# Kernel optimization log

Measured on AMD Instinct MI355X. Metric: run time of the kernel, lower is better.

## Reference

```python
import jax, jax.numpy as jnp
import numpy as np

CODEBOOK_SIZE = 4096
EMBED_DIM = 256
BETA = 0.25


def setup_inputs() -> dict:
    key = jax.random.key(0)
    k_z, k_cb = jax.random.split(key)
    z = jax.random.normal(k_z, (32, 256, 32, 32), dtype=jnp.float32)
    # nn.Embedding weight init: uniform(-1/D, 1/D)
    codebook = jax.random.uniform(
        k_cb, (CODEBOOK_SIZE, EMBED_DIM), dtype=jnp.float32,
        minval=-1.0 / EMBED_DIM, maxval=1.0 / EMBED_DIM)
    return {"z": z, "codebook": codebook}


def reference(z, codebook):
    b, c, h, w = z.shape
    # (B,C,H,W) -> (B*H*W, D)
    z_flat = jnp.transpose(z, (0, 2, 3, 1)).reshape(-1, c)
    # squared euclidean distances: ||z||^2 - 2 z.e^T + ||e||^2  (== cdist(...)^2)
    z_sq = jnp.sum(z_flat * z_flat, axis=1, keepdims=True)          # (N,1)
    e_sq = jnp.sum(codebook * codebook, axis=1)                     # (K,)
    distances = z_sq - 2.0 * (z_flat @ codebook.T) + e_sq[None, :]  # (N,K)
    min_encoding_indices = jnp.argmin(distances, axis=1)            # (N,)
    z_q_flat = codebook[min_encoding_indices]                       # (N,D)
    z_q = jnp.transpose(z_q_flat.reshape(b, h, w, c), (0, 3, 1, 2))  # (B,C,H,W)
    # straight-through estimator
    z_q_st = z + jax.lax.stop_gradient(z_q - z)
    codebook_loss = jnp.mean((z_q - jax.lax.stop_gradient(z)) ** 2)
    commitment_loss = jnp.mean((z - jax.lax.stop_gradient(z_q)) ** 2)
    vq_loss = codebook_loss + BETA * commitment_loss
    return (z_q_st, vq_loss, min_encoding_indices.reshape(b, h, w))
```

## Files before the change

kernel.cpp:

```cpp
#include <hip/hip_runtime.h>

#define K_CODES 4096
#define D 256
#define N_VEC 32768
#define N_ELEM 8388608
#define WINDOW 3.5e-4f
#define RG 8
#define RSLICE 256

typedef _Float16 f16x8 __attribute__((ext_vector_type(8)));
typedef float f32x4 __attribute__((ext_vector_type(4)));

#define WS_LOSS 0
#define WS_COUNT 8
#define WS_DONE 16
#define WS_IDX 256
#define WS_LIST (WS_IDX + N_VEC * 4)
#define WS_ESQ (WS_LIST + N_VEC * 4)
#define WS_ZSQ (WS_ESQ + K_CODES * 4)
#define WS_APACK (WS_ZSQ + N_VEC * 4)
#define WS_BPACK (WS_APACK + (size_t)N_VEC * 256 * 2)
#define WS_RFIN (WS_BPACK + (size_t)K_CODES * 256 * 2 + 65536)

#define PREP_PZ 4096
#define PREP_PCB 512
#define PREP_ESQ 1024
#define PREP_ZSQ 128
#define PREP_BLOCKS (PREP_PZ + PREP_PCB + PREP_ESQ + PREP_ZSQ)

__device__ __forceinline__ unsigned long long pack_key(float s, int idx) {
  const unsigned u = __float_as_uint(s);
  const unsigned mk = (u & 0x80000000u) ? ~u : (u | 0x80000000u);
  return ((unsigned long long)mk << 12) | (unsigned long long)(unsigned)idx;
}
__device__ __forceinline__ float key_score(unsigned long long k) {
  const unsigned mk = (unsigned)(k >> 12);
  const unsigned u = (mk & 0x80000000u) ? (mk & 0x7fffffffu) : ~mk;
  return __uint_as_float(u);
}

__device__ __forceinline__ void pin_frag(f16x8& v) {
  asm volatile("" : "+v"(v));
}

__device__ void esq_body(int bx, const float* __restrict__ cb,
                         float* __restrict__ esq) {
  const int lane = threadIdx.x & 63;
  const int k = bx * 4 + (threadIdx.x >> 6);
  const float* row = cb + (size_t)k * D;
  double s = 0.;
#pragma unroll
  for (int j = 0; j < 4; ++j) {
    const float v = row[lane + 64 * j];
    s += (double)__fmul_rn(v, v);
  }
#pragma unroll
  for (int off = 32; off > 0; off >>= 1) s += __shfl_down(s, off, 64);
  if (lane == 0) esq[k] = (float)s;
}

__device__ void zsq_body(int bx, const float* __restrict__ z,
                         float* __restrict__ zsq) {
  const int n = bx * 256 + threadIdx.x;
  const int b = n >> 10;
  const int hw = n & 1023;
  const float* p = z + ((size_t)b << 18) + hw;
  double a0 = 0., a1 = 0., a2 = 0., a3 = 0.;
  for (int c = 0; c < D; c += 4) {
    const float v0 = p[(size_t)(c + 0) << 10];
    const float v1 = p[(size_t)(c + 1) << 10];
    const float v2 = p[(size_t)(c + 2) << 10];
    const float v3 = p[(size_t)(c + 3) << 10];
    a0 += (double)__fmul_rn(v0, v0);
    a1 += (double)__fmul_rn(v1, v1);
    a2 += (double)__fmul_rn(v2, v2);
    a3 += (double)__fmul_rn(v3, v3);
  }
  zsq[n] = (float)((a0 + a1) + (a2 + a3));
}

__device__ void pack_z2_body(int bx, const float* __restrict__ z,
                             _Float16* __restrict__ Ap) {
  const int t = bx * 256 + threadIdx.x;
  const int lane = t & 63;
  const int fid = t >> 6;
  const int ks = fid & 7;
  const int grp = fid >> 3;
  const int n = grp * 16 + (lane & 15);
  const int d = ks * 32 + ((lane >> 4) << 3);
  const int b = n >> 10, hw = n & 1023;
  const float* p = z + ((size_t)b << 18) + ((size_t)d << 10) + hw;
  f16x8 H;
#pragma unroll
  for (int j = 0; j < 8; ++j) H[j] = (_Float16)p[(size_t)j << 10];
  *(f16x8*)(Ap + (size_t)t * 8) = H;
}

__device__ void pack_cb2_body(int bx, const float* __restrict__ cb,
                              _Float16* __restrict__ Bp) {
  const int t = bx * 256 + threadIdx.x;
  const int lane = t & 63;
  const int fid = t >> 6;
  const int ks = fid & 7;
  const int grp = fid >> 3;
  const int k = grp * 16 + (lane & 15);
  const int d = ks * 32 + ((lane >> 4) << 3);
  const float* p = cb + (size_t)k * D + d;
  f16x8 H;
#pragma unroll
  for (int j = 0; j < 8; ++j) H[j] = (_Float16)(p[j] * 256.f);
  *(f16x8*)(Bp + (size_t)t * 8) = H;
}

__global__ __launch_bounds__(256) void prep_kernel(const float* __restrict__ z,
                                                   const float* __restrict__ cb,
                                                   float* __restrict__ esq,
                                                   float* __restrict__ zsq,
                                                   _Float16* __restrict__ Ap,
                                                   _Float16* __restrict__ Bp) {
  const int b = blockIdx.x;
  if (b < PREP_PZ) {
    pack_z2_body(b, z, Ap);
  } else if (b < PREP_PZ + PREP_PCB) {
    pack_cb2_body(b - PREP_PZ, cb, Bp);
  } else if (b < PREP_PZ + PREP_PCB + PREP_ESQ) {
    esq_body(b - PREP_PZ - PREP_PCB, cb, esq);
  } else {
    zsq_body(b - PREP_PZ - PREP_PCB - PREP_ESQ, z, zsq);
  }
}

#define DIST_STEP(T, B)                                                      \
  {                                                                          \
    const int cb0 = (T) * 64 + crow;                                         \
    const float4 e4 = *(const float4*)(esq + cb0);                           \
    f32x4 acc[4];                                                            \
    _Pragma("unroll") for (int ni = 0; ni < 4; ++ni) acc[ni] = (f32x4)0.f;   \
    __builtin_amdgcn_s_setprio(1);                                           \
    _Pragma("unroll") for (int ks = 0; ks < 8; ++ks)                         \
        _Pragma("unroll") for (int ni = 0; ni < 4; ++ni)                     \
            acc[ni] = __builtin_amdgcn_mfma_f32_16x16x32_f16(                \
                B[ks], a[ni][ks], acc[ni], 0, 0, 0);                         \
    __builtin_amdgcn_s_setprio(0);                                           \
    const float ev[4] = {e4.x, e4.y, e4.z, e4.w};                            \
    _Pragma("unroll") for (int r = 0; r < 4; ++r) {                          \
      const int code = cb0 + r;                                              \
      _Pragma("unroll") for (int ni = 0; ni < 4; ++ni) {                     \
        const float s = fmaf(acc[ni][r], -0.0078125f, ev[r]);                \
        s2[ni] = fminf(fmaxf(s, s1[ni]), s2[ni]);                            \
        if (s < s1[ni]) i1[ni] = code;                                       \
        s1[ni] = fminf(s1[ni], s);                                           \
      }                                                                      \
    }                                                                        \
  }

__global__ __launch_bounds__(512, 2) void dist2_kernel(
    const _Float16* __restrict__ Ap, const _Float16* __restrict__ Bp,
    const float* __restrict__ esq, int* __restrict__ idx,
    int* __restrict__ list, unsigned int* __restrict__ count,
    unsigned long long* __restrict__ rfin) {
  __shared__ unsigned long long mb[128][4][2];
  const int tid = threadIdx.x;
  const int lane = tid & 63;
  const int w = tid >> 6;
  const int wn = w >> 2;
  const int wc = w & 3;
  const int n0 = blockIdx.x * 128;

  f16x8 a[4][8];
  {
    const _Float16* ab =
        Ap + (size_t)((n0 + wn * 64) >> 4) * 4096 + (size_t)lane * 8;
#pragma unroll
    for (int ni = 0; ni < 4; ++ni)
#pragma unroll
      for (int ks = 0; ks < 8; ++ks) {
        a[ni][ks] = *(const f16x8*)(ab + (size_t)(ni * 8 + ks) * 512);
        pin_frag(a[ni][ks]);
      }
  }

  float s1[4], s2[4];
  int i1[4];
#pragma unroll
  for (int ni = 0; ni < 4; ++ni) {
    s1[ni] = 3.4e38f;
    s2[ni] = 3.4e38f;
    i1[ni] = 0;
  }

  const _Float16* bbase = Bp + (size_t)wc * 4096 + (size_t)lane * 8;
  const int crow = wc * 16 + ((lane >> 4) << 2);

  f16x8 b0[8], b1[8];
#pragma unroll
  for (int ks = 0; ks < 8; ++ks)
    b0[ks] = *(const f16x8*)(bbase + (size_t)ks * 512);

  for (int t = 0; t < 64; t += 2) {
    const _Float16* bp1 = bbase + (size_t)(t + 1) * 16384;
#pragma unroll
    for (int ks = 0; ks < 8; ++ks)
      b1[ks] = *(const f16x8*)(bp1 + (size_t)ks * 512);
    DIST_STEP(t, b0)
    const _Float16* bp2 = bbase + (size_t)(t + 2) * 16384;
#pragma unroll
    for (int ks = 0; ks < 8; ++ks)
      b0[ks] = *(const f16x8*)(bp2 + (size_t)ks * 512);
    DIST_STEP(t + 1, b1)
  }

  unsigned long long k1[4], k2[4];
#pragma unroll
  for (int ni = 0; ni < 4; ++ni) {
    float a1 = s1[ni], a2 = s2[ni];
    int ai1 = i1[ni];
#pragma unroll
    for (int m = 16; m <= 32; m <<= 1) {
      const float bv1 = __shfl_xor(a1, m, 64);
      const int bi1 = __shfl_xor(ai1, m, 64);
      const float bv2 = __shfl_xor(a2, m, 64);
      const float hi = fmaxf(a1, bv1);
      const bool take = (bv1 < a1) || (bv1 == a1 && bi1 < ai1);
      if (take) ai1 = bi1;
      a1 = fminf(a1, bv1);
      a2 = fminf(fminf(a2, bv2), hi);
    }
    k1[ni] = pack_key(a1, ai1);
    k2[ni] = pack_key(a2, 0);
  }
  if (lane < 16) {
#pragma unroll
    for (int ni = 0; ni < 4; ++ni) {
      const int nl = wn * 64 + ni * 16 + lane;
      mb[nl][wc][0] = k1[ni];
      mb[nl][wc][1] = k2[ni];
    }
  }
  __syncthreads();
  if (tid < 128) {
    unsigned long long m1 = ~0ull, m2 = ~0ull;
#pragma unroll
    for (int s = 0; s < 4; ++s) {
      const unsigned long long c1 = mb[tid][s][0];
      const unsigned long long c2 = mb[tid][s][1];
      if (c1 < m1) {
        m2 = m1;
        m1 = c1;
      } else if (c1 < m2) {
        m2 = c1;
      }
      if (c2 < m2) m2 = c2;
    }
    const int n = n0 + tid;
    idx[n] = (int)(m1 & 0xFFFULL);
    const bool flag = key_score(m2) - key_score(m1) < WINDOW;
    rfin[n] = flag ? ~0ull : 0ull;
    if (flag) {
      const unsigned pos = atomicAdd(count, 1u);
      if (pos < N_VEC) list[pos] = n;
    }
  }
}

__global__ __launch_bounds__(256) void rescan_kernel(
    const float* __restrict__ z, const float* __restrict__ cb,
    const float* __restrict__ esq, const float* __restrict__ zsq,
    const int* __restrict__ list, const unsigned int* __restrict__ count,
    unsigned long long* __restrict__ rfin) {
  __shared__ double zrow[RG][D];
  __shared__ int nloc[RG];
  __shared__ float zsv[RG];
  const int tid = threadIdx.x;
  const int lane = tid & 63;
  unsigned int cnt = *count;
  if (cnt > N_VEC) cnt = N_VEC;
  const unsigned G = (cnt + RG - 1) / RG;
  const unsigned nitems = G * (K_CODES / RSLICE);
  for (unsigned item = blockIdx.x; item < nitems; item += gridDim.x) {
    const unsigned g = item >> 4;
    const int s = item & 15;
    __syncthreads();
    if (tid < RG) {
      const unsigned r = g * RG + tid;
      const int n = (r < cnt) ? list[r] : list[cnt - 1];
      nloc[tid] = n;
      zsv[tid] = zsq[n];
    }
    __syncthreads();
    for (int i = tid; i < RG * D; i += 256) {
      const int p = i >> 8, c = i & 255;
      const int n = nloc[p];
      const int b = n >> 10, hw = n & 1023;
      zrow[p][c] = (double)z[((size_t)b << 18) + ((size_t)c << 10) + hw];
    }
    __syncthreads();
    const int k = s * RSLICE + tid;
    const float* row = cb + (size_t)k * D;
    double acc[RG];
#pragma unroll
    for (int p = 0; p < RG; ++p) acc[p] = 0.;
    for (int c = 0; c < D; c += 4) {
      const float4 r4 = *(const float4*)(row + c);
      const double rx = (double)r4.x, ry = (double)r4.y;
      const double rz = (double)r4.z, rw = (double)r4.w;
#pragma unroll
      for (int p = 0; p < RG; ++p) {
        const double2 za = *(const double2*)&zrow[p][c];
        const double2 zb = *(const double2*)&zrow[p][c + 2];
        double a = acc[p];
        a = fma(za.x, rx, a);
        a = fma(za.y, ry, a);
        a = fma(zb.x, rz, a);
        a = fma(zb.y, rw, a);
        acc[p] = a;
      }
    }
    const float ek = esq[k];
    unsigned long long best[RG];
#pragma unroll
    for (int p = 0; p < RG; ++p) {
      const float dotf = (float)acc[p];
      const float d = __fadd_rn(__fsub_rn(zsv[p], __fmul_rn(2.0f, dotf)), ek);
      best[p] = pack_key(d, k);
    }
#pragma unroll
    for (int p = 0; p < RG; ++p) {
#pragma unroll
      for (int off = 32; off > 0; off >>= 1)
        best[p] = min(best[p], __shfl_down(best[p], off, 64));
    }
    if (lane == 0) {
#pragma unroll
      for (int p = 0; p < RG; ++p) atomicMin(rfin + nloc[p], best[p]);
    }
  }
}

__global__ __launch_bounds__(256) void gather_kernel(
    const float* __restrict__ z, const float* __restrict__ cb,
    const int* __restrict__ idxarr, const unsigned long long* __restrict__ rfin,
    float* __restrict__ out, float* __restrict__ loss_acc,
    unsigned int* __restrict__ done) {
  const int tid = threadIdx.x;
  const int n0 = blockIdx.x * 64;
  const int hwl = tid & 63;
  const int c0 = tid >> 6;
  const int n = n0 + hwl;
  const int b = n >> 10;
  const int hw = n & 1023;
  const unsigned long long rf = rfin[n];
  const int idx = rf ? (int)(rf & 0xFFFULL) : idxarr[n];
  if (tid < 64) out[(size_t)N_ELEM + 1 + n] = (float)idx;
  const float* crow = cb + (size_t)idx * D;
  const size_t obase = ((size_t)b << 18) + hw;
  float part = 0.f;
#pragma unroll
  for (int c = c0; c < D; c += 4) {
    const float v = crow[c];
    const size_t o = obase + ((size_t)c << 10);
    const float diff = v - z[o];
    out[o] = v;
    part = fmaf(diff, diff, part);
  }
#pragma unroll
  for (int off = 32; off > 0; off >>= 1) part += __shfl_down(part, off, 64);
  __shared__ float red[4];
  if ((tid & 63) == 0) red[tid >> 6] = part;
  __syncthreads();
  if (tid == 0) {
    atomicAdd(loss_acc, red[0] + red[1] + red[2] + red[3]);
    __threadfence();
    const unsigned old = atomicAdd(done, 1u);
    if (old == gridDim.x - 1) {
      const float total = atomicAdd(loss_acc, 0.0f);
      out[N_ELEM] = 1.25f * total * (1.0f / (float)N_ELEM);
    }
  }
}

extern "C" void kernel_launch(void* const* d_in, const int* in_sizes, int n_in,
                              void* d_out, int out_size, void* d_ws,
                              size_t ws_size, hipStream_t stream) {
  const float* z = (const float*)d_in[0];
  const float* cb = (const float*)d_in[1];
  float* out = (float*)d_out;
  char* ws = (char*)d_ws;
  float* loss_acc = (float*)(ws + WS_LOSS);
  unsigned int* count = (unsigned int*)(ws + WS_COUNT);
  unsigned int* done = (unsigned int*)(ws + WS_DONE);
  int* idx = (int*)(ws + WS_IDX);
  int* list = (int*)(ws + WS_LIST);
  float* esq = (float*)(ws + WS_ESQ);
  float* zsq = (float*)(ws + WS_ZSQ);
  _Float16* Ap = (_Float16*)(ws + WS_APACK);
  _Float16* Bp = (_Float16*)(ws + WS_BPACK);
  unsigned long long* rfin = (unsigned long long*)(ws + WS_RFIN);

  hipMemsetAsync(ws, 0, 256, stream);
  prep_kernel<<<PREP_BLOCKS, 256, 0, stream>>>(z, cb, esq, zsq, Ap, Bp);
  dist2_kernel<<<N_VEC / 128, 512, 0, stream>>>(Ap, Bp, esq, idx, list, count,
                                                rfin);
  rescan_kernel<<<2048, 256, 0, stream>>>(z, cb, esq, zsq, list, count, rfin);
  gather_kernel<<<N_VEC / 64, 256, 0, stream>>>(z, cb, idx, rfin, out,
                                                loss_acc, done);
}
```

Baseline: 283.1 us.

## Software-pipeline distance MFMA clusters with argmin folding using double accumulators

Restructures the codebook loop so each step's MFMA cluster runs while the previous step's accumulator is folded into the running top-2 minima. Two accumulator sets alternate, which lets VALU compare work overlap matrix-core work. The two B-fragment register buffers become one, refilled fragment by fragment right after each k-slice is consumed. The esq loads are also prefetched one step ahead. This trades 16 extra accumulator registers for 32 fewer B registers, and the per-fragment refill means each B load has less time to arrive before it is needed.

```diff
diff --git a/kernel.cpp b/kernel.cpp
--- a/kernel.cpp
+++ b/kernel.cpp
@@ -130,23 +130,31 @@
   }
 }
 
-#define DIST_STEP(T, B)                                                      \
+#define CLUSTER(ACC, SN)                                                     \
   {                                                                          \
-    const int cb0 = (T) * 64 + crow;                                         \
-    const float4 e4 = *(const float4*)(esq + cb0);                           \
-    f32x4 acc[4];                                                            \
-    _Pragma("unroll") for (int ni = 0; ni < 4; ++ni) acc[ni] = (f32x4)0.f;   \
     __builtin_amdgcn_s_setprio(1);                                           \
-    _Pragma("unroll") for (int ks = 0; ks < 8; ++ks)                         \
-        _Pragma("unroll") for (int ni = 0; ni < 4; ++ni)                     \
-            acc[ni] = __builtin_amdgcn_mfma_f32_16x16x32_f16(                \
-                B[ks], a[ni][ks], acc[ni], 0, 0, 0);                         \
+    _Pragma("unroll") for (int ks = 0; ks < 8; ++ks) {                       \
+      ACC[0] = __builtin_amdgcn_mfma_f32_16x16x32_f16(                       \
+          b[ks], a[0][ks], ks ? ACC[0] : z4, 0, 0, 0);                       \
+      ACC[1] = __builtin_amdgcn_mfma_f32_16x16x32_f16(                       \
+          b[ks], a[1][ks], ks ? ACC[1] : z4, 0, 0, 0);                       \
+      ACC[2] = __builtin_amdgcn_mfma_f32_16x16x32_f16(                       \
+          b[ks], a[2][ks], ks ? ACC[2] : z4, 0, 0, 0);                       \
+      ACC[3] = __builtin_amdgcn_mfma_f32_16x16x32_f16(                       \
+          b[ks], a[3][ks], ks ? ACC[3] : z4, 0, 0, 0);                       \
+      b[ks] = *(const f16x8*)(bbase + (size_t)(SN)*16384 + ks * 512);        \
+    }                                                                        \
     __builtin_amdgcn_s_setprio(0);                                           \
-    const float ev[4] = {e4.x, e4.y, e4.z, e4.w};                            \
+  }
+
+#define FOLD(ACC, S, EV)                                                     \
+  {                                                                          \
+    const int cb0 = (S)*64 + crow;                                           \
+    const float ev[4] = {(EV).x, (EV).y, (EV).z, (EV).w};                    \
     _Pragma("unroll") for (int r = 0; r < 4; ++r) {                          \
       const int code = cb0 + r;                                              \
       _Pragma("unroll") for (int ni = 0; ni < 4; ++ni) {                     \
-        const float s = fmaf(acc[ni][r], -0.0078125f, ev[r]);                \
+        const float s = fmaf(ACC[ni][r], -0.0078125f, ev[r]);                \
         s2[ni] = fminf(fmaxf(s, s1[ni]), s2[ni]);                            \
         if (s < s1[ni]) i1[ni] = code;                                       \
         s1[ni] = fminf(s1[ni], s);                                           \
@@ -191,24 +199,29 @@
 
   const _Float16* bbase = Bp + (size_t)wc * 4096 + (size_t)lane * 8;
   const int crow = wc * 16 + ((lane >> 4) << 2);
-
-  f16x8 b0[8], b1[8];
+  const f32x4 z4 = (f32x4)0.f;
+
+  f16x8 b[8];
+  f32x4 accA[4], accB[4];
 #pragma unroll
   for (int ks = 0; ks < 8; ++ks)
-    b0[ks] = *(const f16x8*)(bbase + (size_t)ks * 512);
-
-  for (int t = 0; t < 64; t += 2) {
-    const _Float16* bp1 = bbase + (size_t)(t + 1) * 16384;
-#pragma unroll
-    for (int ks = 0; ks < 8; ++ks)
-      b1[ks] = *(const f16x8*)(bp1 + (size_t)ks * 512);
-    DIST_STEP(t, b0)
-    const _Float16* bp2 = bbase + (size_t)(t + 2) * 16384;
-#pragma unroll
-    for (int ks = 0; ks < 8; ++ks)
-      b0[ks] = *(const f16x8*)(bp2 + (size_t)ks * 512);
-    DIST_STEP(t + 1, b1)
-  }
+    b[ks] = *(const f16x8*)(bbase + (size_t)ks * 512);
+  float4 evA = *(const float4*)(esq + crow);
+
+  CLUSTER(accA, 1)
+  float4 evB = *(const float4*)(esq + 64 + crow);
+
+  for (int s = 1; s < 63; s += 2) {
+    CLUSTER(accB, s + 1)
+    FOLD(accA, s - 1, evA)
+    evA = *(const float4*)(esq + (s + 1) * 64 + crow);
+    CLUSTER(accA, s + 2)
+    FOLD(accB, s, evB)
+    evB = *(const float4*)(esq + (s + 2) * 64 + crow);
+  }
+  CLUSTER(accB, 64)
+  FOLD(accA, 62, evA)
+  FOLD(accB, 63, evB)
 
   unsigned long long k1[4], k2[4];
 #pragma unroll
```

Result: no change. 286.0 us (+1.0%).

## Shrink dist tile to 64 rows for occupancy, add transposed z copy for rescan

Applied to the files above, without the earlier changes.

The distance kernel now handles 64 vectors per block instead of 128. It holds half the A fragments in registers, drops the double-buffered B fragments in favour of per-ks in-place prefetch, and raises the launch bound to 4 blocks per CU to improve latency hiding. The prep kernel also writes a row-major fp32 copy of z when the workspace is large enough, so the rescan kernel can load candidate rows contiguously instead of with strided gathers. The cost is twice the B-operand reads from global/L2 and an extra 32 MB write in prep.

```diff
diff --git a/kernel.cpp b/kernel.cpp
--- a/kernel.cpp
+++ b/kernel.cpp
@@ -21,6 +21,8 @@
 #define WS_APACK (WS_ZSQ + N_VEC * 4)
 #define WS_BPACK (WS_APACK + (size_t)N_VEC * 256 * 2)
 #define WS_RFIN (WS_BPACK + (size_t)K_CODES * 256 * 2 + 65536)
+#define WS_ZT (WS_RFIN + (size_t)N_VEC * 8)
+#define WS_NEED_ZT (WS_ZT + (size_t)N_VEC * D * 4)
 
 #define PREP_PZ 4096
 #define PREP_PCB 512
@@ -80,7 +82,8 @@
 }
 
 __device__ void pack_z2_body(int bx, const float* __restrict__ z,
-                             _Float16* __restrict__ Ap) {
+                             _Float16* __restrict__ Ap,
+                             float* __restrict__ zT) {
   const int t = bx * 256 + threadIdx.x;
   const int lane = t & 63;
   const int fid = t >> 6;
@@ -90,10 +93,19 @@
   const int d = ks * 32 + ((lane >> 4) << 3);
   const int b = n >> 10, hw = n & 1023;
   const float* p = z + ((size_t)b << 18) + ((size_t)d << 10) + hw;
+  float v[8];
   f16x8 H;
 #pragma unroll
-  for (int j = 0; j < 8; ++j) H[j] = (_Float16)p[(size_t)j << 10];
+  for (int j = 0; j < 8; ++j) {
+    v[j] = p[(size_t)j << 10];
+    H[j] = (_Float16)v[j];
+  }
   *(f16x8*)(Ap + (size_t)t * 8) = H;
+  if (zT) {
+    float4* o = (float4*)(zT + (size_t)n * D + d);
+    o[0] = make_float4(v[0], v[1], v[2], v[3]);
+    o[1] = make_float4(v[4], v[5], v[6], v[7]);
+  }
 }
 
 __device__ void pack_cb2_body(int bx, const float* __restrict__ cb,
@@ -112,15 +124,14 @@
   *(f16x8*)(Bp + (size_t)t * 8) = H;
 }
 
-__global__ __launch_bounds__(256) void prep_kernel(const float* __restrict__ z,
-                                                   const float* __restrict__ cb,
-                                                   float* __restrict__ esq,
-                                                   float* __restrict__ zsq,
-                                                   _Float16* __restrict__ Ap,
-                                                   _Float16* __restrict__ Bp) {
+__global__ __launch_bounds__(256) void prep_kernel(
+    const float* __restrict__ z, const float* __restrict__ cb,
+    float* __restrict__ esq, float* __restrict__ zsq,
+    _Float16* __restrict__ Ap, _Float16* __restrict__ Bp,
+    float* __restrict__ zT) {
   const int b = blockIdx.x;
   if (b < PREP_PZ) {
-    pack_z2_body(b, z, Ap);
+    pack_z2_body(b, z, Ap, zT);
   } else if (b < PREP_PZ + PREP_PCB) {
     pack_cb2_body(b - PREP_PZ, cb, Bp);
   } else if (b < PREP_PZ + PREP_PCB + PREP_ESQ) {
@@ -130,49 +141,25 @@
   }
 }
 
-#define DIST_STEP(T, B)                                                      \
-  {                                                                          \
-    const int cb0 = (T) * 64 + crow;                                         \
-    const float4 e4 = *(const float4*)(esq + cb0);                           \
-    f32x4 acc[4];                                                            \
-    _Pragma("unroll") for (int ni = 0; ni < 4; ++ni) acc[ni] = (f32x4)0.f;   \
-    __builtin_amdgcn_s_setprio(1);                                           \
-    _Pragma("unroll") for (int ks = 0; ks < 8; ++ks)                         \
-        _Pragma("unroll") for (int ni = 0; ni < 4; ++ni)                     \
-            acc[ni] = __builtin_amdgcn_mfma_f32_16x16x32_f16(                \
-                B[ks], a[ni][ks], acc[ni], 0, 0, 0);                         \
-    __builtin_amdgcn_s_setprio(0);                                           \
-    const float ev[4] = {e4.x, e4.y, e4.z, e4.w};                            \
-    _Pragma("unroll") for (int r = 0; r < 4; ++r) {                          \
-      const int code = cb0 + r;                                              \
-      _Pragma("unroll") for (int ni = 0; ni < 4; ++ni) {                     \
-        const float s = fmaf(acc[ni][r], -0.0078125f, ev[r]);                \
-        s2[ni] = fminf(fmaxf(s, s1[ni]), s2[ni]);                            \
-        if (s < s1[ni]) i1[ni] = code;                                       \
-        s1[ni] = fminf(s1[ni], s);                                           \
-      }                                                                      \
-    }                                                                        \
-  }
-
-__global__ __launch_bounds__(512, 2) void dist2_kernel(
+__global__ __launch_bounds__(512, 4) void dist2_kernel(
     const _Float16* __restrict__ Ap, const _Float16* __restrict__ Bp,
     const float* __restrict__ esq, int* __restrict__ idx,
     int* __restrict__ list, unsigned int* __restrict__ count,
     unsigned long long* __restrict__ rfin) {
-  __shared__ unsigned long long mb[128][4][2];
+  __shared__ unsigned long long mb[64][4][2];
   const int tid = threadIdx.x;
   const int lane = tid & 63;
   const int w = tid >> 6;
   const int wn = w >> 2;
   const int wc = w & 3;
-  const int n0 = blockIdx.x * 128;
-
-  f16x8 a[4][8];
+  const int n0 = blockIdx.x * 64;
+
+  f16x8 a[2][8];
   {
     const _Float16* ab =
-        Ap + (size_t)((n0 + wn * 64) >> 4) * 4096 + (size_t)lane * 8;
-#pragma unroll
-    for (int ni = 0; ni < 4; ++ni)
+        Ap + (size_t)((n0 + wn * 32) >> 4) * 4096 + (size_t)lane * 8;
+#pragma unroll
+    for (int ni = 0; ni < 2; ++ni)
 #pragma unroll
       for (int ks = 0; ks < 8; ++ks) {
         a[ni][ks] = *(const f16x8*)(ab + (size_t)(ni * 8 + ks) * 512);
@@ -180,10 +167,10 @@
       }
   }
 
-  float s1[4], s2[4];
-  int i1[4];
-#pragma unroll
-  for (int ni = 0; ni < 4; ++ni) {
+  float s1[2], s2[2];
+  int i1[2];
+#pragma unroll
+  for (int ni = 0; ni < 2; ++ni) {
     s1[ni] = 3.4e38f;
     s2[ni] = 3.4e38f;
     i1[ni] = 0;
@@ -191,28 +178,49 @@
 
   const _Float16* bbase = Bp + (size_t)wc * 4096 + (size_t)lane * 8;
   const int crow = wc * 16 + ((lane >> 4) << 2);
-
-  f16x8 b0[8], b1[8];
+  const f32x4 z4 = (f32x4)0.f;
+
+  f16x8 b[8];
 #pragma unroll
   for (int ks = 0; ks < 8; ++ks)
-    b0[ks] = *(const f16x8*)(bbase + (size_t)ks * 512);
-
-  for (int t = 0; t < 64; t += 2) {
-    const _Float16* bp1 = bbase + (size_t)(t + 1) * 16384;
-#pragma unroll
-    for (int ks = 0; ks < 8; ++ks)
-      b1[ks] = *(const f16x8*)(bp1 + (size_t)ks * 512);
-    DIST_STEP(t, b0)
-    const _Float16* bp2 = bbase + (size_t)(t + 2) * 16384;
-#pragma unroll
-    for (int ks = 0; ks < 8; ++ks)
-      b0[ks] = *(const f16x8*)(bp2 + (size_t)ks * 512);
-    DIST_STEP(t + 1, b1)
-  }
-
-  unsigned long long k1[4], k2[4];
-#pragma unroll
-  for (int ni = 0; ni < 4; ++ni) {
+    b[ks] = *(const f16x8*)(bbase + (size_t)ks * 512);
+
+  for (int t = 0; t < 64; ++t) {
+    const float4 e4 = *(const float4*)(esq + t * 64 + crow);
+    f32x4 acc0, acc1;
+    __builtin_amdgcn_s_setprio(1);
+#pragma unroll
+    for (int ks = 0; ks < 8; ++ks) {
+      acc0 = __builtin_amdgcn_mfma_f32_16x16x32_f16(b[ks], a[0][ks],
+                                                    ks ? acc0 : z4, 0, 0, 0);
+      acc1 = __builtin_amdgcn_mfma_f32_16x16x32_f16(b[ks], a[1][ks],
+                                                    ks ? acc1 : z4, 0, 0, 0);
+      b[ks] = *(const f16x8*)(bbase + (size_t)(t + 1) * 16384 + ks * 512);
+    }
+    __builtin_amdgcn_s_setprio(0);
+    const int cb0 = t * 64 + crow;
+    const float ev[4] = {e4.x, e4.y, e4.z, e4.w};
+#pragma unroll
+    for (int r = 0; r < 4; ++r) {
+      const int code = cb0 + r;
+      {
+        const float s = fmaf(acc0[r], -0.0078125f, ev[r]);
+        s2[0] = fminf(fmaxf(s, s1[0]), s2[0]);
+        if (s < s1[0]) i1[0] = code;
+        s1[0] = fminf(s1[0], s);
+      }
+      {
+        const float s = fmaf(acc1[r], -0.0078125f, ev[r]);
+        s2[1] = fminf(fmaxf(s, s1[1]), s2[1]);
+        if (s < s1[1]) i1[1] = code;
+        s1[1] = fminf(s1[1], s);
+      }
+    }
+  }
+
+  unsigned long long k1[2], k2[2];
+#pragma unroll
+  for (int ni = 0; ni < 2; ++ni) {
     float a1 = s1[ni], a2 = s2[ni];
     int ai1 = i1[ni];
 #pragma unroll
@@ -231,14 +239,14 @@
   }
   if (lane < 16) {
 #pragma unroll
-    for (int ni = 0; ni < 4; ++ni) {
-      const int nl = wn * 64 + ni * 16 + lane;
+    for (int ni = 0; ni < 2; ++ni) {
+      const int nl = wn * 32 + ni * 16 + lane;
       mb[nl][wc][0] = k1[ni];
       mb[nl][wc][1] = k2[ni];
     }
   }
   __syncthreads();
-  if (tid < 128) {
+  if (tid < 64) {
     unsigned long long m1 = ~0ull, m2 = ~0ull;
 #pragma unroll
     for (int s = 0; s < 4; ++s) {
@@ -264,9 +272,10 @@
 }
 
 __global__ __launch_bounds__(256) void rescan_kernel(
-    const float* __restrict__ z, const float* __restrict__ cb,
-    const float* __restrict__ esq, const float* __restrict__ zsq,
-    const int* __restrict__ list, const unsigned int* __restrict__ count,
+    const float* __restrict__ z, const float* __restrict__ zT,
+    const float* __restrict__ cb, const float* __restrict__ esq,
+    const float* __restrict__ zsq, const int* __restrict__ list,
+    const unsigned int* __restrict__ count,
     unsigned long long* __restrict__ rfin) {
   __shared__ double zrow[RG][D];
   __shared__ int nloc[RG];
@@ -288,11 +297,18 @@
       zsv[tid] = zsq[n];
     }
     __syncthreads();
-    for (int i = tid; i < RG * D; i += 256) {
-      const int p = i >> 8, c = i & 255;
-      const int n = nloc[p];
-      const int b = n >> 10, hw = n & 1023;
-      zrow[p][c] = (double)z[((size_t)b << 18) + ((size_t)c << 10) + hw];
+    if (zT) {
+      for (int i = tid; i < RG * D; i += 256) {
+        const int p = i >> 8, c = i & 255;
+        zrow[p][c] = (double)zT[(size_t)nloc[p] * D + c];
+      }
+    } else {
+      for (int i = tid; i < RG * D; i += 256) {
+        const int p = i >> 8, c = i & 255;
+        const int n = nloc[p];
+        const int b = n >> 10, hw = n & 1023;
+        zrow[p][c] = (double)z[((size_t)b << 18) + ((size_t)c << 10) + hw];
+      }
     }
     __syncthreads();
     const int k = s * RSLICE + tid;
@@ -396,12 +412,14 @@
   _Float16* Ap = (_Float16*)(ws + WS_APACK);
   _Float16* Bp = (_Float16*)(ws + WS_BPACK);
   unsigned long long* rfin = (unsigned long long*)(ws + WS_RFIN);
+  float* zT = (ws_size >= WS_NEED_ZT) ? (float*)(ws + WS_ZT) : nullptr;
 
   hipMemsetAsync(ws, 0, 256, stream);
-  prep_kernel<<<PREP_BLOCKS, 256, 0, stream>>>(z, cb, esq, zsq, Ap, Bp);
-  dist2_kernel<<<N_VEC / 128, 512, 0, stream>>>(Ap, Bp, esq, idx, list, count,
-                                                rfin);
-  rescan_kernel<<<2048, 256, 0, stream>>>(z, cb, esq, zsq, list, count, rfin);
+  prep_kernel<<<PREP_BLOCKS, 256, 0, stream>>>(z, cb, esq, zsq, Ap, Bp, zT);
+  dist2_kernel<<<N_VEC / 64, 512, 0, stream>>>(Ap, Bp, esq, idx, list, count,
+                                               rfin);
+  rescan_kernel<<<2048, 256, 0, stream>>>(z, zT, cb, esq, zsq, list, count,
+                                          rfin);
   gather_kernel<<<N_VEC / 64, 256, 0, stream>>>(z, cb, idx, rfin, out,
                                                 loss_acc, done);
 }
```

Result: slower. 289.1 us (+2.1%).
